# Performance work log

Measured on AMD Instinct MI355X. Metric: run time of the kernel, lower is better.

Reference implementation:

```python
import jax, jax.numpy as jnp
import numpy as np
import math

D_MODEL = 1024
NUM_HEADS = 16
BATCH = 4
SEQ = 2048

def setup_inputs() -> dict:
    key = jax.random.key(0)
    ks = jax.random.split(key, 7)
    s = 1.0 / math.sqrt(D_MODEL)
    return {
        "x": jax.random.normal(ks[0], (BATCH, SEQ, D_MODEL), dtype=jnp.float32),
        "Wq": jax.random.normal(ks[1], (D_MODEL, D_MODEL), dtype=jnp.float32) * s,
        "bq": jax.random.normal(ks[2], (D_MODEL,), dtype=jnp.float32) * s,
        "Wk": jax.random.normal(ks[3], (D_MODEL, D_MODEL), dtype=jnp.float32) * s,
        "bk": jax.random.normal(ks[4], (D_MODEL,), dtype=jnp.float32) * s,
        "Wv": jax.random.normal(ks[5], (D_MODEL, D_MODEL), dtype=jnp.float32) * s,
        "bv": jax.random.normal(ks[6], (D_MODEL,), dtype=jnp.float32) * s,
        "num_heads": NUM_HEADS,
    }

def reference(x, Wq, bq, Wk, bk, Wv, bv, num_heads):
    B, S, D = x.shape
    hd = D // num_heads
    scale = 1.0 / math.sqrt(D)  # NOTE: module scales by sqrt(d_model), not sqrt(head_dim)
    # torch nn.Linear: y = x @ W.T + b
    q = x @ Wq.T + bq
    k = x @ Wk.T + bk
    v = x @ Wv.T + bv
    # Faithful replication of the module's (non-standard) row-major view:
    # (B, S, D) -> (B*H, S, D/H)
    q = q.reshape(B * num_heads, -1, hd)
    k = k.reshape(B * num_heads, -1, hd)
    v = v.reshape(B * num_heads, -1, hd)
    scores = jnp.einsum('bqd,bkd->bqk', q, k) * scale  # [B*H, S, S]
    probs = jax.nn.softmax(scores, axis=-1)
    out = jnp.einsum('bqk,bkd->bqd', probs, v)
    return out.reshape(B, -1, D)
```

## Files before the change

### kernel.cpp

```cpp
#include <hip/hip_runtime.h>
#include <stdint.h>

typedef unsigned short u16;
typedef __attribute__((ext_vector_type(8))) short short8;
typedef __attribute__((ext_vector_type(4))) float f32x4;
typedef __attribute__((ext_vector_type(16))) float f32x16;
typedef __attribute__((ext_vector_type(2))) unsigned int uv2;
typedef __attribute__((ext_vector_type(4))) unsigned int uv4;

#define MFMA16(a, b, c) __builtin_amdgcn_mfma_f32_16x16x32_bf16((a), (b), (c), 0, 0, 0)
#define MFMA32(a, b, c) __builtin_amdgcn_mfma_f32_32x32x16_bf16((a), (b), (c), 0, 0, 0)
#define LOG2E 1.4426950408889634f
#define SCALE 0.03125f
#define KC (SCALE * LOG2E)

__device__ __forceinline__ u16 f2bf(float f) {
  union { float f; uint32_t u; } cv; cv.f = f;
  uint32_t u = cv.u;
  uint32_t r = (u + 0x7fffu + ((u >> 16) & 1u)) >> 16;
  return (u16)r;
}

__device__ __forceinline__ unsigned cvtpk(float lo, float hi) {
  unsigned r;
  asm("v_cvt_pk_bf16_f32 %0, %1, %2" : "=v"(r) : "v"(lo), "v"(hi));
  return r;
}

__device__ __forceinline__ void gld(const void* g, void* l) {
  __builtin_amdgcn_global_load_lds(
      (const __attribute__((address_space(1))) void*)g,
      (__attribute__((address_space(3))) void*)l, 16, 0, 0);
}

__device__ __forceinline__ const short8* tile8(const u16* base, int row, int c) {
  return (const short8*)(base + row * 64 + (((c) ^ (row & 7)) << 3));
}

__global__ void cvt4_kernel(const float* __restrict__ x, const float* __restrict__ wq,
                            const float* __restrict__ wk, const float* __restrict__ wv,
                            u16* __restrict__ xb, u16* __restrict__ wqb,
                            u16* __restrict__ wkb, u16* __restrict__ wvb) {
  const int NX8 = 1048576;
  const int NW8 = 131072;
  const int TOT = NX8 + 3 * NW8;
  int i = blockIdx.x * blockDim.x + threadIdx.x;
  const int stride = gridDim.x * blockDim.x;
  for (; i < TOT; i += stride) {
    const float* src; u16* dst; int j;
    if (i < NX8) { src = x; dst = xb; j = i; }
    else if (i < NX8 + NW8) { src = wq; dst = wqb; j = i - NX8; }
    else if (i < NX8 + 2 * NW8) { src = wk; dst = wkb; j = i - NX8 - NW8; }
    else { src = wv; dst = wvb; j = i - NX8 - 2 * NW8; }
    const f32x4* s = (const f32x4*)src + (size_t)j * 2;
    f32x4 a = s[0], b = s[1];
    short8 o;
    o[0] = (short)f2bf(a[0]); o[1] = (short)f2bf(a[1]);
    o[2] = (short)f2bf(a[2]); o[3] = (short)f2bf(a[3]);
    o[4] = (short)f2bf(b[0]); o[5] = (short)f2bf(b[1]);
    o[6] = (short)f2bf(b[2]); o[7] = (short)f2bf(b[3]);
    *((short8*)dst + j) = o;
  }
}

__global__ __launch_bounds__(256) void gemm_qkv(
    const u16* __restrict__ xb,
    const u16* __restrict__ wqb, const u16* __restrict__ wkb, const u16* __restrict__ wvb,
    const float* __restrict__ bq, const float* __restrict__ bk, const float* __restrict__ bv,
    u16* __restrict__ qo, u16* __restrict__ ko, u16* __restrict__ vo) {
  __shared__ __align__(16) u16 sm[2][128 * 64];

  const int bid = blockIdx.x;
  const int cx = bid & 7, qq = bid >> 3;
  const int m = ((qq & 7) << 3) + cx;
  const int nz = qq >> 3;
  const int n = nz / 3;
  const int z = nz - n * 3;
  const u16* W = (z == 0) ? wqb : (z == 1) ? wkb : wvb;
  const float* bias = (z == 0) ? bq : (z == 1) ? bk : bv;
  u16* out = (z == 0) ? qo : (z == 1) ? ko : vo;
  const float oscale = (z == 0) ? KC : 1.0f;
  const int m0 = m * 128, n0 = n * 128;

  const int t = threadIdx.x;
  const int lane = t & 63;
  const int w = t >> 6;
  const int l15 = lane & 15, l4 = lane >> 4;
  const int mw = (w >> 1) * 64, nw = (w & 1) * 64;

  const int srow8 = lane >> 3;
  const int ssw = ((lane & 7) ^ srow8) << 3;
  const u16* aG = xb + (size_t)(m0 + (w * 4) * 8 + srow8) * 1024 + ssw;
  const u16* bG = W + (size_t)(n0 + (w * 4) * 8 + srow8) * 1024 + ssw;
  u16* aL = &sm[0][0] + (w * 4) * 512 + lane * 8;
  u16* bL = &sm[1][0] + (w * 4) * 512 + lane * 8;

  float biasv[4];
#pragma unroll
  for (int nj = 0; nj < 4; nj++) biasv[nj] = bias[n0 + nw + nj * 16 + l15];

  const f32x4 fz = {0.f, 0.f, 0.f, 0.f};
  f32x4 acc[4][4];
#pragma unroll
  for (int i = 0; i < 4; i++)
#pragma unroll
    for (int j = 0; j < 4; j++) acc[i][j] = fz;

  for (int k0 = 0; k0 < 1024; k0 += 64) {
    __syncthreads();
#pragma unroll
    for (int cc = 0; cc < 4; cc++) {
      gld(aG + k0 + (size_t)cc * 8 * 1024, aL + cc * 512);
      gld(bG + k0 + (size_t)cc * 8 * 1024, bL + cc * 512);
    }
    __syncthreads();
#pragma unroll
    for (int kk = 0; kk < 2; kk++) {
      short8 af[4], bf[4];
#pragma unroll
      for (int mi = 0; mi < 4; mi++) af[mi] = *tile8(&sm[0][0], mw + mi * 16 + l15, kk * 4 + l4);
#pragma unroll
      for (int nj = 0; nj < 4; nj++) bf[nj] = *tile8(&sm[1][0], nw + nj * 16 + l15, kk * 4 + l4);
      __builtin_amdgcn_s_setprio(1);
#pragma unroll
      for (int mi = 0; mi < 4; mi++)
#pragma unroll
        for (int nj = 0; nj < 4; nj++)
          acc[mi][nj] = MFMA16(af[mi], bf[nj], acc[mi][nj]);
      __builtin_amdgcn_s_setprio(0);
    }
  }

  __syncthreads();
  u16* Cs = &sm[0][0] + w * 4096;
#pragma unroll
  for (int mi = 0; mi < 4; mi++)
#pragma unroll
    for (int nj = 0; nj < 4; nj++)
#pragma unroll
      for (int r = 0; r < 4; r++) {
        const int row = mi * 16 + l4 * 4 + r;
        const int col = nj * 16 + l15;
        Cs[row * 64 + (((col >> 3) ^ (row & 7)) << 3) + (col & 7)] =
            f2bf((acc[mi][nj][r] + biasv[nj]) * oscale);
      }
#pragma unroll
  for (int i = 0; i < 8; i++) {
    const int row = i * 8 + (lane >> 3);
    short8 vv = *tile8(Cs, row, lane & 7);
    *(short8*)(out + (size_t)(m0 + mw + row) * 1024 + n0 + nw + (lane & 7) * 8) = vv;
  }
}

__global__ void repack_kv(const u16* __restrict__ k, const u16* __restrict__ v,
                          u16* __restrict__ kpk, u16* __restrict__ vpk) {
  __shared__ __align__(16) u16 LK[4096];
  __shared__ u16 LV[4096];
  const int g = blockIdx.y, tt = blockIdx.x;
  const size_t sb = (size_t)g * 131072 + (size_t)tt * 4096;
  const int t = threadIdx.x;
#pragma unroll
  for (int i = 0; i < 2; i++) {
    const int ccc = t + i * 256;
    const int r = ccc >> 3, d0 = (ccc & 7) * 8;
    short8 dk = *(const short8*)(k + sb + (size_t)r * 64 + d0);
    const int b = r >> 5, ks = d0 >> 4;
    const int L = (r & 31) | (((d0 >> 3) & 1) << 5);
    *(short8*)(LK + ((b * 4 + ks) << 9) + L * 8) = dk;
    short8 dv = *(const short8*)(v + sb + (size_t)r * 64 + d0);
    const int c = r >> 3, j = r & 7;
    const int h2 = d0 >> 5;
    const int base = h2 * 2048 + (c >> 1) * 512 + (c & 1) * 256 + j;
#pragma unroll
    for (int jj = 0; jj < 8; jj++) LV[base + ((d0 & 31) + jj) * 8] = (u16)dv[jj];
  }
  __syncthreads();
#pragma unroll
  for (int i = 0; i < 2; i++) {
    const int ccc = t + i * 256;
    *(short8*)(kpk + sb + ccc * 8) = *(const short8*)(LK + ccc * 8);
    *(short8*)(vpk + sb + ccc * 8) = *(const short8*)(LV + ccc * 8);
  }
}


__device__ __forceinline__ void qblock(f32x16& s, float& lsum, f32x16& o0, f32x16& o1,
                                       const short8* vf) {
  float p[16];
  float ps = 0.f;
#pragma unroll
  for (int i = 0; i < 16; i++) {
    p[i] = __builtin_amdgcn_exp2f(s[i]);
    ps += p[i];
  }
  lsum += ps;

  short8 pa0, pa1;
  {
    unsigned a0 = cvtpk(p[0], p[1]);
    unsigned a1 = cvtpk(p[2], p[3]);
    unsigned b0 = cvtpk(p[4], p[5]);
    unsigned b1 = cvtpk(p[6], p[7]);
    uv2 r0 = __builtin_amdgcn_permlane32_swap(a0, b0, false, false);
    uv2 r1 = __builtin_amdgcn_permlane32_swap(a1, b1, false, false);
    union { uv4 u; short8 s8; } cc;
    cc.u[0] = r0[0]; cc.u[1] = r1[0]; cc.u[2] = r0[1]; cc.u[3] = r1[1];
    pa0 = cc.s8;
  }
  {
    unsigned a0 = cvtpk(p[8], p[9]);
    unsigned a1 = cvtpk(p[10], p[11]);
    unsigned b0 = cvtpk(p[12], p[13]);
    unsigned b1 = cvtpk(p[14], p[15]);
    uv2 r0 = __builtin_amdgcn_permlane32_swap(a0, b0, false, false);
    uv2 r1 = __builtin_amdgcn_permlane32_swap(a1, b1, false, false);
    union { uv4 u; short8 s8; } cc;
    cc.u[0] = r0[0]; cc.u[1] = r1[0]; cc.u[2] = r0[1]; cc.u[3] = r1[1];
    pa1 = cc.s8;
  }
  __builtin_amdgcn_s_setprio(1);
  o0 = MFMA32(pa0, vf[0], o0);
  o0 = MFMA32(pa1, vf[1], o0);
  o1 = MFMA32(pa0, vf[2], o1);
  o1 = MFMA32(pa1, vf[3], o1);
  __builtin_amdgcn_s_setprio(0);
}

__global__ __launch_bounds__(256, 4) void attn_kernel(const u16* __restrict__ q,
                                                      const u16* __restrict__ kpk,
                                                      const u16* __restrict__ vpk,
                                                      float* __restrict__ out) {
  __shared__ __align__(16) u16 Ks[2][4096];
  const int t = threadIdx.x, lane = t & 63, w = t >> 6;
  const int l31 = lane & 31, hi = lane >> 5;
  const int bid = blockIdx.x;
  const int cx = bid & 7, qq = bid >> 3;
  const int qt = qq & 15;
  const int g = ((qq >> 4) << 3) + cx;
  const size_t gb = (size_t)g * 131072;
  const int q0 = qt * 128 + w * 32;

  const u16* qp = q + gb + (size_t)(q0 + l31) * 64 + hi * 8;
  short8 qf[4];
#pragma unroll
  for (int ks = 0; ks < 4; ks++) qf[ks] = *(const short8*)(qp + ks * 16);

  const u16* kS = kpk + gb + w * 1024 + (size_t)lane * 8;
  const u16* vP = vpk + gb + (size_t)lane * 8;
  const u16* kR0 = &Ks[0][0] + lane * 8;
  const u16* kR1 = &Ks[1][0] + lane * 8;

  f32x16 o0, o1;
#pragma unroll
  for (int i = 0; i < 16; i++) { o0[i] = 0.f; o1[i] = 0.f; }
  float lsum = 0.f;

  {
    u16* kD = &Ks[0][0] + w * 1024 + lane * 8;
    gld(kS, kD);
    gld(kS + 512, kD + 512);
  }
  __syncthreads();

  for (int tt = 0; tt < 32; ++tt) {
    const int cur = tt & 1;
    if (tt < 31) {
      u16* kD = (cur ? &Ks[0][0] : &Ks[1][0]) + w * 1024 + lane * 8;
      const u16* kSn = kS + (size_t)(tt + 1) * 4096;
      gld(kSn, kD);
      gld(kSn + 512, kD + 512);
    }
    const u16* kR = cur ? kR1 : kR0;
    const u16* vT = vP + (size_t)tt * 4096;
#pragma unroll
    for (int b = 0; b < 2; b++) {
      short8 vf[4];
      vf[0] = *(const short8*)(vT + (b << 1) * 512);
      vf[1] = *(const short8*)(vT + ((b << 1) | 1) * 512);
      vf[2] = *(const short8*)(vT + 2048 + (b << 1) * 512);
      vf[3] = *(const short8*)(vT + 2048 + ((b << 1) | 1) * 512);
      short8 kf[4];
#pragma unroll
      for (int ks = 0; ks < 4; ks++)
        kf[ks] = *(const short8*)(kR + ((b << 2) | ks) * 512);
      f32x16 s;
#pragma unroll
      for (int i = 0; i < 16; i++) s[i] = 0.f;
      __builtin_amdgcn_s_setprio(1);
#pragma unroll
      for (int ks = 0; ks < 4; ks++) s = MFMA32(kf[ks], qf[ks], s);
      __builtin_amdgcn_s_setprio(0);
      qblock(s, lsum, o0, o1, vf);
    }
    __syncthreads();
  }

  float lt = lsum + __shfl_xor(lsum, 32);
  float inv = 1.0f / lt;
  float* ob = out + gb + (size_t)q0 * 64;
#pragma unroll
  for (int r = 0; r < 16; r++) {
    int qr = (r & 3) + 8 * (r >> 2) + 4 * hi;
    float ir = __shfl(inv, qr);
    ob[(size_t)qr * 64 + l31] = o0[r] * ir;
    ob[(size_t)qr * 64 + 32 + l31] = o1[r] * ir;
  }
}

extern "C" void kernel_launch(void* const* d_in, const int* in_sizes, int n_in,
                              void* d_out, int out_size, void* d_ws, size_t ws_size,
                              hipStream_t stream) {
  const float* x  = (const float*)d_in[0];
  const float* Wq = (const float*)d_in[1];
  const float* bq = (const float*)d_in[2];
  const float* Wk = (const float*)d_in[3];
  const float* bk = (const float*)d_in[4];
  const float* Wv = (const float*)d_in[5];
  const float* bv = (const float*)d_in[6];
  float* out = (float*)d_out;

  const size_t NX = 8388608;
  const size_t NW = 1048576;
  u16* ws = (u16*)d_ws;
  u16* xb  = ws;
  u16* wqb = xb + NX;
  u16* wkb = wqb + NW;
  u16* wvb = wkb + NW;
  u16* qb  = wvb + NW;
  u16* kb  = qb + NX;
  u16* vb  = kb + NX;
  u16* vpk = vb + NX;
  u16* kpk = xb;

  cvt4_kernel<<<2048, 256, 0, stream>>>(x, Wq, Wk, Wv, xb, wqb, wkb, wvb);

  gemm_qkv<<<1536, 256, 0, stream>>>(xb, wqb, wkb, wvb, bq, bk, bv, qb, kb, vb);

  repack_kv<<<dim3(32, 64), 256, 0, stream>>>(kb, vb, kpk, vpk);

  attn_kernel<<<1024, 256, 0, stream>>>(qb, kpk, vpk, out);
}
```

Measured before the change: 157.8 us.

## Split attention KV range in two halves and combine partial outputs

Splits each attention block's key/value loop into two halves, launching twice as many blocks that each write unnormalized bf16 partial outputs and row sums, then adds a combine kernel that sums the halves and normalizes. The aim is more blocks in flight to fill the GPU better (1024 blocks at 4 per CU is under one wave). The split skips max-subtraction merging, which relies on the existing softmax having no running max. It costs an extra kernel launch, partial-output memory traffic, and bf16 rounding of the unnormalized partial accumulators.

```diff
diff --git a/kernel.cpp b/kernel.cpp
--- a/kernel.cpp
+++ b/kernel.cpp
@@ -19,6 +19,11 @@
   uint32_t u = cv.u;
   uint32_t r = (u + 0x7fffu + ((u >> 16) & 1u)) >> 16;
   return (u16)r;
+}
+
+__device__ __forceinline__ float bf2f(u16 b) {
+  union { uint32_t u; float f; } cv; cv.u = ((uint32_t)b) << 16;
+  return cv.f;
 }
 
 __device__ __forceinline__ unsigned cvtpk(float lo, float hi) {
@@ -229,24 +234,29 @@
 __global__ __launch_bounds__(256, 4) void attn_kernel(const u16* __restrict__ q,
                                                       const u16* __restrict__ kpk,
                                                       const u16* __restrict__ vpk,
-                                                      float* __restrict__ out) {
+                                                      u16* __restrict__ oA,
+                                                      u16* __restrict__ oB,
+                                                      float* __restrict__ lA,
+                                                      float* __restrict__ lB) {
   __shared__ __align__(16) u16 Ks[2][4096];
   const int t = threadIdx.x, lane = t & 63, w = t >> 6;
   const int l31 = lane & 31, hi = lane >> 5;
   const int bid = blockIdx.x;
   const int cx = bid & 7, qq = bid >> 3;
-  const int qt = qq & 15;
-  const int g = ((qq >> 4) << 3) + cx;
+  const int h = qq & 1;
+  const int qt = (qq >> 1) & 15;
+  const int g = ((qq >> 5) << 3) + cx;
   const size_t gb = (size_t)g * 131072;
   const int q0 = qt * 128 + w * 32;
+  const size_t hb = (size_t)h * 16 * 4096;
 
   const u16* qp = q + gb + (size_t)(q0 + l31) * 64 + hi * 8;
   short8 qf[4];
 #pragma unroll
   for (int ks = 0; ks < 4; ks++) qf[ks] = *(const short8*)(qp + ks * 16);
 
-  const u16* kS = kpk + gb + w * 1024 + (size_t)lane * 8;
-  const u16* vP = vpk + gb + (size_t)lane * 8;
+  const u16* kS = kpk + gb + hb + w * 1024 + (size_t)lane * 8;
+  const u16* vP = vpk + gb + hb + (size_t)lane * 8;
   const u16* kR0 = &Ks[0][0] + lane * 8;
   const u16* kR1 = &Ks[1][0] + lane * 8;
 
@@ -262,9 +272,9 @@
   }
   __syncthreads();
 
-  for (int tt = 0; tt < 32; ++tt) {
+  for (int tt = 0; tt < 16; ++tt) {
     const int cur = tt & 1;
-    if (tt < 31) {
+    if (tt < 15) {
       u16* kD = (cur ? &Ks[0][0] : &Ks[1][0]) + w * 1024 + lane * 8;
       const u16* kSn = kS + (size_t)(tt + 1) * 4096;
       gld(kSn, kD);
@@ -296,14 +306,34 @@
   }
 
   float lt = lsum + __shfl_xor(lsum, 32);
-  float inv = 1.0f / lt;
-  float* ob = out + gb + (size_t)q0 * 64;
+  u16* po = (h ? oB : oA) + gb + (size_t)q0 * 64;
 #pragma unroll
   for (int r = 0; r < 16; r++) {
     int qr = (r & 3) + 8 * (r >> 2) + 4 * hi;
-    float ir = __shfl(inv, qr);
-    ob[(size_t)qr * 64 + l31] = o0[r] * ir;
-    ob[(size_t)qr * 64 + 32 + l31] = o1[r] * ir;
+    po[(size_t)qr * 64 + l31] = f2bf(o0[r]);
+    po[(size_t)qr * 64 + 32 + l31] = f2bf(o1[r]);
+  }
+  if (hi == 0) (h ? lB : lA)[g * 2048 + q0 + l31] = lt;
+}
+
+__global__ void combine_kernel(float* __restrict__ out, const u16* __restrict__ oA,
+                               const u16* __restrict__ oB, const float* __restrict__ lA,
+                               const float* __restrict__ lB) {
+  int i = blockIdx.x * blockDim.x + threadIdx.x;
+  const int stride = gridDim.x * blockDim.x;
+  for (; i < 1048576; i += stride) {
+    const int row = i >> 3;
+    const float inv = 1.0f / (lA[row] + lB[row]);
+    short8 a = ((const short8*)oA)[i];
+    short8 b = ((const short8*)oB)[i];
+    f32x4 r0, r1;
+#pragma unroll
+    for (int j = 0; j < 4; j++) {
+      r0[j] = (bf2f((u16)a[j]) + bf2f((u16)b[j])) * inv;
+      r1[j] = (bf2f((u16)a[4 + j]) + bf2f((u16)b[4 + j])) * inv;
+    }
+    ((f32x4*)out)[i * 2] = r0;
+    ((f32x4*)out)[i * 2 + 1] = r1;
   }
 }
 
@@ -332,11 +362,18 @@
   u16* vpk = vb + NX;
   u16* kpk = xb;
 
+  u16* oA = kb;
+  u16* oB = vb;
+  float* lA = (float*)wqb;
+  float* lB = (float*)wkb;
+
   cvt4_kernel<<<2048, 256, 0, stream>>>(x, Wq, Wk, Wv, xb, wqb, wkb, wvb);
 
   gemm_qkv<<<1536, 256, 0, stream>>>(xb, wqb, wkb, wvb, bq, bk, bv, qb, kb, vb);
 
   repack_kv<<<dim3(32, 64), 256, 0, stream>>>(kb, vb, kpk, vpk);
 
-  attn_kernel<<<1024, 256, 0, stream>>>(qb, kpk, vpk, out);
-}
+  attn_kernel<<<2048, 256, 0, stream>>>(qb, kpk, vpk, oA, oB, lA, lB);
+
+  combine_kernel<<<1024, 256, 0, stream>>>(out, oA, oB, lA, lB);
+}
```

New measurement: 169.4 us. 7.3% more time.

## Triple-buffer K tiles in LDS with two-ahead prefetch and partial vmcnt waits

Applied to the files above, without the earlier changes.

Changes the K shared-memory staging from double to triple buffering. Loads are now issued two tiles ahead, and each iteration ends with a partial s_waitcnt vmcnt plus a raw s_barrier instead of a full __syncthreads, so the load for the next-next tile stays in flight across the barrier. The first QK MFMA now takes a hoisted zero accumulator instead of zeroing s each iteration. This costs an extra 8 KB of LDS per block, which may reduce occupancy at 4 blocks per CU. It also relies on hand-managed vmcnt counts being correct, and the V global loads in the same loop also count toward vmcnt.

```diff
diff --git a/kernel.cpp b/kernel.cpp
--- a/kernel.cpp
+++ b/kernel.cpp
@@ -230,7 +230,7 @@
                                                       const u16* __restrict__ kpk,
                                                       const u16* __restrict__ vpk,
                                                       float* __restrict__ out) {
-  __shared__ __align__(16) u16 Ks[2][4096];
+  __shared__ __align__(16) u16 Ks[3][4096];
   const int t = threadIdx.x, lane = t & 63, w = t >> 6;
   const int l31 = lane & 31, hi = lane >> 5;
   const int bid = blockIdx.x;
@@ -247,30 +247,28 @@
 
   const u16* kS = kpk + gb + w * 1024 + (size_t)lane * 8;
   const u16* vP = vpk + gb + (size_t)lane * 8;
-  const u16* kR0 = &Ks[0][0] + lane * 8;
-  const u16* kR1 = &Ks[1][0] + lane * 8;
+  const int ldOff = w * 1024 + lane * 8;
+  const int rdOff = lane * 8;
 
   f32x16 o0, o1;
 #pragma unroll
   for (int i = 0; i < 16; i++) { o0[i] = 0.f; o1[i] = 0.f; }
   float lsum = 0.f;
-
-  {
-    u16* kD = &Ks[0][0] + w * 1024 + lane * 8;
-    gld(kS, kD);
-    gld(kS + 512, kD + 512);
-  }
-  __syncthreads();
-
+  f32x16 Z;
+#pragma unroll
+  for (int i = 0; i < 16; i++) Z[i] = 0.f;
+
+  gld(kS, &Ks[0][0] + ldOff);
+  gld(kS + 512, &Ks[0][0] + ldOff + 512);
+  gld(kS + 4096, &Ks[1][0] + ldOff);
+  gld(kS + 4096 + 512, &Ks[1][0] + ldOff + 512);
+  asm volatile("s_waitcnt vmcnt(2)" ::: "memory");
+  __builtin_amdgcn_s_barrier();
+  __builtin_amdgcn_sched_barrier(0);
+
+  int cur = 0;
   for (int tt = 0; tt < 32; ++tt) {
-    const int cur = tt & 1;
-    if (tt < 31) {
-      u16* kD = (cur ? &Ks[0][0] : &Ks[1][0]) + w * 1024 + lane * 8;
-      const u16* kSn = kS + (size_t)(tt + 1) * 4096;
-      gld(kSn, kD);
-      gld(kSn + 512, kD + 512);
-    }
-    const u16* kR = cur ? kR1 : kR0;
+    const u16* kR = &Ks[cur][0] + rdOff;
     const u16* vT = vP + (size_t)tt * 4096;
 #pragma unroll
     for (int b = 0; b < 2; b++) {
@@ -283,16 +281,31 @@
 #pragma unroll
       for (int ks = 0; ks < 4; ks++)
         kf[ks] = *(const short8*)(kR + ((b << 2) | ks) * 512);
-      f32x16 s;
-#pragma unroll
-      for (int i = 0; i < 16; i++) s[i] = 0.f;
       __builtin_amdgcn_s_setprio(1);
-#pragma unroll
-      for (int ks = 0; ks < 4; ks++) s = MFMA32(kf[ks], qf[ks], s);
+      f32x16 s = MFMA32(kf[0], qf[0], Z);
+      s = MFMA32(kf[1], qf[1], s);
+      s = MFMA32(kf[2], qf[2], s);
+      s = MFMA32(kf[3], qf[3], s);
       __builtin_amdgcn_s_setprio(0);
       qblock(s, lsum, o0, o1, vf);
     }
-    __syncthreads();
+    if (tt < 30) {
+      const int nb = (cur + 2 >= 3) ? cur - 1 : cur + 2;
+      u16* kD = &Ks[nb][0] + ldOff;
+      const u16* kSn = kS + (size_t)(tt + 2) * 4096;
+      gld(kSn, kD);
+      gld(kSn + 512, kD + 512);
+    }
+    if (tt < 31) {
+      if (tt < 30) {
+        asm volatile("s_waitcnt vmcnt(2)" ::: "memory");
+      } else {
+        asm volatile("s_waitcnt vmcnt(0)" ::: "memory");
+      }
+      __builtin_amdgcn_s_barrier();
+      __builtin_amdgcn_sched_barrier(0);
+    }
+    cur = (cur + 1 >= 3) ? 0 : cur + 1;
   }
 
   float lt = lsum + __shfl_xor(lsum, 32);
```

Measured after the change: 158.5 us. No clear change (+0.4%).
